# Optimization experiments

Hardware: AMD Instinct MI355X
Metric: run time of the kernel (lower is better)

## Reference

```python
import jax, jax.numpy as jnp
import numpy as np

B, D_IN, D_DENSE, S1, S2 = 16384, 1024, 1024, 1024, 1024
SPARSITY1, SPARSITY2 = 0.1, 0.01  # fraction of zeros in the 'sparse' weights


def setup_inputs() -> dict:
    key = jax.random.key(0)
    kx, k0, k1, k2, km1, km2 = jax.random.split(key, 6)
    x = jax.random.normal(kx, (B, D_IN), dtype=jnp.float32)
    # dense layer params (nn.Linear): weight [out, in], bias [out]
    w0 = jax.random.normal(k0, (D_DENSE, D_IN), dtype=jnp.float32) / np.sqrt(D_IN)
    b0 = jnp.zeros((D_DENSE,), dtype=jnp.float32)
    # sparse layers: dense randn weight elementwise-masked (mask keeps with prob 1-sparsity)
    w1 = jax.random.normal(k1, (S1, D_DENSE), dtype=jnp.float32)
    mask1 = jax.random.uniform(km1, (S1, D_DENSE)) > SPARSITY1
    b1 = jnp.zeros((S1,), dtype=jnp.float32)
    w2 = jax.random.normal(k2, (S2, S1), dtype=jnp.float32)
    mask2 = jax.random.uniform(km2, (S2, S1)) > SPARSITY2
    b2 = jnp.zeros((S2,), dtype=jnp.float32)
    return {"x": x, "w0": w0, "b0": b0, "w1": w1, "b1": b1, "mask1": mask1,
            "w2": w2, "b2": b2, "mask2": mask2}


def reference(x, w0, b0, w1, b1, mask1, w2, b2, mask2):
    # layer 1: dense linear + ReLU
    h = jax.nn.relu(jnp.einsum('bi,oi->bo', x, w0) + b0)
    # layer 2: masked ('sparse' COO in torch) linear + bias + ReLU
    h = jax.nn.relu(jnp.einsum('bi,oi->bo', h, w1 * mask1) + b1)
    # layer 3: masked linear + bias + ReLU
    out = jax.nn.relu(jnp.einsum('bi,oi->bo', h, w2 * mask2) + b2)
    return out
```

## Files before the change

### kernel.cpp

```cpp
#include <hip/hip_runtime.h>
#include <hip/hip_bf16.h>
#include <cstdint>
#include <cstddef>


typedef __bf16 bf16x8 __attribute__((ext_vector_type(8)));
typedef float  f32x4  __attribute__((ext_vector_type(4)));

#define AS1 __attribute__((address_space(1)))
#define AS3 __attribute__((address_space(3)))

__device__ __forceinline__ void gload_lds16(const void* g, void* l) {
    __builtin_amdgcn_global_load_lds((const AS1 void*)g, (AS3 void*)l, 16, 0, 0);
}

__global__ void detect_mask(const unsigned char* __restrict__ m, int* __restrict__ flag) {
    const int t = threadIdx.x;
    int or1 = 0, or3 = 0;
    for (int e = t; e < 256; e += 64) { or1 |= m[e * 4 + 1]; or3 |= m[e * 4 + 3]; }
    unsigned long long b1 = __ballot(or1 != 0);
    unsigned long long b3 = __ballot(or3 != 0);
    if (t == 0) *flag = b1 ? 1 : (b3 ? 2 : 0);
}

__device__ __forceinline__ void prep_body(const float* __restrict__ w,
                                          const void* __restrict__ mask, int mode,
                                          __bf16* __restrict__ out, long i) {
    float4 a = *reinterpret_cast<const float4*>(w + i);
    float4 b = *reinterpret_cast<const float4*>(w + i + 4);
    float v[8] = {a.x, a.y, a.z, a.w, b.x, b.y, b.z, b.w};
    if (mask) {
        if (mode == 1) {
            const unsigned char* mp = (const unsigned char*)mask;
            #pragma unroll
            for (int j = 0; j < 8; ++j) v[j] = mp[i + j] ? v[j] : 0.f;
        } else if (mode == 0) {
            const int* mp = (const int*)mask;
            #pragma unroll
            for (int j = 0; j < 8; ++j) v[j] = mp[i + j] ? v[j] : 0.f;
        } else {
            const float* mp = (const float*)mask;
            #pragma unroll
            for (int j = 0; j < 8; ++j) v[j] = (mp[i + j] != 0.f) ? v[j] : 0.f;
        }
    }
    bf16x8 o;
    #pragma unroll
    for (int j = 0; j < 8; ++j) o[j] = (__bf16)v[j];
    *reinterpret_cast<bf16x8*>(out + i) = o;
}

__global__ void prep_all(const float* __restrict__ x, __bf16* __restrict__ xb,
                         const float* __restrict__ w0, const float* __restrict__ w1,
                         const float* __restrict__ w2,
                         const void* __restrict__ m1, const void* __restrict__ m2,
                         const int* __restrict__ flag,
                         __bf16* __restrict__ w0b, __bf16* __restrict__ w1b,
                         __bf16* __restrict__ w2b) {
    const int bid = blockIdx.x;
    if (bid < 8192) {
        long i = ((long)bid * blockDim.x + threadIdx.x) * 8;
        float4 a = *reinterpret_cast<const float4*>(x + i);
        float4 b = *reinterpret_cast<const float4*>(x + i + 4);
        bf16x8 o;
        o[0] = (__bf16)a.x; o[1] = (__bf16)a.y; o[2] = (__bf16)a.z; o[3] = (__bf16)a.w;
        o[4] = (__bf16)b.x; o[5] = (__bf16)b.y; o[6] = (__bf16)b.z; o[7] = (__bf16)b.w;
        *reinterpret_cast<bf16x8*>(xb + i) = o;
    } else {
        const int q = bid - 8192, wi = q >> 9, sub = q & 511;
        long i = ((long)sub * blockDim.x + threadIdx.x) * 8;
        const int mode = *flag;
        if (wi == 0)      prep_body(w0, nullptr, mode, w0b, i);
        else if (wi == 1) prep_body(w1, m1,      mode, w1b, i);
        else              prep_body(w2, m2,      mode, w2b, i);
    }
}

__device__ __forceinline__ f32x4 mfma16(bf16x8 a, bf16x8 b, f32x4 c) {
    return __builtin_amdgcn_mfma_f32_16x16x32_bf16(a, b, c, 0, 0, 0);
}

#define MFMAQ(Q, A00, A01, A10, A11)                                        \
    __builtin_amdgcn_s_setprio(1);                                          \
    _Pragma("unroll")                                                       \
    for (int n = 0; n < 4; ++n) {                                           \
        acc[2*(Q)][n]   = mfma16(A00, b[n][0], acc[2*(Q)][n]);              \
        acc[2*(Q)][n]   = mfma16(A01, b[n][1], acc[2*(Q)][n]);              \
        acc[2*(Q)+1][n] = mfma16(A10, b[n][0], acc[2*(Q)+1][n]);            \
        acc[2*(Q)+1][n] = mfma16(A11, b[n][1], acc[2*(Q)+1][n]);            \
    }                                                                       \
    __builtin_amdgcn_s_setprio(0);

#define BAR()   __builtin_amdgcn_s_barrier(); __builtin_amdgcn_sched_barrier(0)
#define LGKM0() asm volatile("s_waitcnt lgkmcnt(0)" ::: "memory")
#define VM8()   asm volatile("s_waitcnt vmcnt(8)" ::: "memory")
#define VM0()   asm volatile("s_waitcnt vmcnt(0)" ::: "memory")

template<bool F32OUT>
__global__ __launch_bounds__(512, 2) void gemm8p(
    const __bf16* __restrict__ A, const __bf16* __restrict__ W,
    const float* __restrict__ bias,
    __bf16* __restrict__ outb, float* __restrict__ outf) {
    constexpr int NT = 16;
    extern __shared__ char smem[];

    const int t   = threadIdx.x;
    const int l   = t & 63, l15 = l & 15, lhi = l >> 4;
    const int w   = t >> 6, wr = w >> 2, wc = w & 3;

    const int bid = blockIdx.x;
    const int swz = (bid & 7) * 32 + (bid >> 3);
    const int bx = swz & 3, by = swz >> 2;
    const int brow = by * 256, bcol = bx * 256;

    const int srow = t >> 3;
    const int scol = (((t & 7) ^ ((t >> 3) & 7)) << 4) >> 1;
    const __bf16* gA = A + (size_t)(brow + srow) * 1024 + scol;
    const __bf16* gW = W + (size_t)(bcol + srow) * 1024 + scol;
    const int woff = (t & 448) * 16;

    char* const ldsA = smem;
    char* const ldsB = smem + 65536;

    auto stageAfull = [&](int d, int k0) {
        const __bf16* g = gA + k0;
        char* p = ldsA + d * 32768 + woff;
        gload_lds16(g,          p);
        gload_lds16(g + 65536,  p + 8192);
        gload_lds16(g + 131072, p + 16384);
        gload_lds16(g + 196608, p + 24576);
    };
    auto stageBh = [&](int d, int h, int k0) {
        const __bf16* g = gW + (size_t)h * 131072 + k0;
        char* p = ldsB + d * 32768 + h * 16384 + woff;
        gload_lds16(g, p);
        gload_lds16(g + 65536, p + 8192);
    };

    const int xorm  = (l & 7) << 4;
    const int koff0 = (lhi * 16) ^ xorm;
    const int koff1 = (64 + lhi * 16) ^ xorm;
    char* const aBase = ldsA + wr * 16384 + l15 * 128;
    char* const bBase = ldsB + wc * 8192 + l15 * 128;

    f32x4 acc[8][4] = {};

    stageAfull(0, 0);  stageBh(0, 0, 0);  stageBh(0, 1, 0);
    stageAfull(1, 64); stageBh(1, 0, 64); stageBh(1, 1, 64);
    VM8(); BAR();

    #pragma unroll 2
    for (int tt = 0; tt < NT; ++tt) {
        const int d  = tt & 1;
        const int k2 = (tt + 2) * 64;
        char* const aB = aBase + d * 32768;
        char* const bB = bBase + d * 32768;
        const bool st = (tt + 2 < NT);

        bf16x8 b[4][2];
        #pragma unroll
        for (int n = 0; n < 4; ++n) {
            b[n][0] = *(const bf16x8*)(bB + n * 2048 + koff0);
            b[n][1] = *(const bf16x8*)(bB + n * 2048 + koff1);
        }
        bf16x8 a00 = *(const bf16x8*)(aB + 0 * 2048 + koff0);
        bf16x8 a01 = *(const bf16x8*)(aB + 0 * 2048 + koff1);
        bf16x8 a10 = *(const bf16x8*)(aB + 1 * 2048 + koff0);
        bf16x8 a11 = *(const bf16x8*)(aB + 1 * 2048 + koff1);
        bf16x8 c00 = *(const bf16x8*)(aB + 2 * 2048 + koff0);
        bf16x8 c01 = *(const bf16x8*)(aB + 2 * 2048 + koff1);
        bf16x8 c10 = *(const bf16x8*)(aB + 3 * 2048 + koff0);
        bf16x8 c11 = *(const bf16x8*)(aB + 3 * 2048 + koff1);
        MFMAQ(0, a00, a01, a10, a11);
        LGKM0(); BAR();

        if (st) stageBh(d, 0, k2);
        a00 = *(const bf16x8*)(aB + 4 * 2048 + koff0);
        a01 = *(const bf16x8*)(aB + 4 * 2048 + koff1);
        a10 = *(const bf16x8*)(aB + 5 * 2048 + koff0);
        a11 = *(const bf16x8*)(aB + 5 * 2048 + koff1);
        MFMAQ(1, c00, c01, c10, c11);
        LGKM0(); BAR();

        if (st) stageBh(d, 1, k2);
        c00 = *(const bf16x8*)(aB + 6 * 2048 + koff0);
        c01 = *(const bf16x8*)(aB + 6 * 2048 + koff1);
        c10 = *(const bf16x8*)(aB + 7 * 2048 + koff0);
        c11 = *(const bf16x8*)(aB + 7 * 2048 + koff1);
        MFMAQ(2, a00, a01, a10, a11);
        LGKM0(); BAR();

        if (st) stageAfull(d, k2);
        MFMAQ(3, c00, c01, c10, c11);
        if (tt <= NT - 3)      { VM8(); BAR(); }
        else if (tt == NT - 2) { VM0(); BAR(); }
    }

    if constexpr (F32OUT) {
        const int orow = brow + wr * 128 + lhi * 4;
        const int ocol = bcol + wc * 64 + l15;
        #pragma unroll
        for (int n = 0; n < 4; ++n) {
            const int col = ocol + n * 16;
            const float bv = bias[col];
            #pragma unroll
            for (int m = 0; m < 8; ++m) {
                const int r0 = orow + m * 16;
                #pragma unroll
                for (int r = 0; r < 4; ++r) {
                    float v = acc[m][n][r] + bv;
                    outf[(size_t)(r0 + r) * 1024 + col] = v > 0.f ? v : 0.f;
                }
            }
        }
    } else {
        __syncthreads();
        char* const cl = smem;
        #pragma unroll
        for (int n = 0; n < 4; ++n) {
            const int colb = (wc * 64 + n * 16 + l15) * 2;
            const float bv = bias[bcol + wc * 64 + n * 16 + l15];
            #pragma unroll
            for (int m = 0; m < 8; ++m) {
                #pragma unroll
                for (int r = 0; r < 4; ++r) {
                    const int row = wr * 128 + m * 16 + lhi * 4 + r;
                    float v = acc[m][n][r] + bv;
                    v = v > 0.f ? v : 0.f;
                    *(__bf16*)(cl + row * 512 + (colb ^ ((row & 12) << 3))) = (__bf16)v;
                }
            }
        }
        __syncthreads();
        #pragma unroll
        for (int rd = 0; rd < 16; ++rd) {
            const int off = rd * 8192 + t * 16;
            const int row = off >> 9;
            const int cb  = (off & 511) ^ ((row & 12) << 3);
            bf16x8 v = *(const bf16x8*)(cl + off);
            *(bf16x8*)((char*)outb + ((size_t)(brow + row) * 1024 + bcol) * 2 + cb) = v;
        }
    }
}

extern "C" void kernel_launch(void* const* d_in, const int* in_sizes, int n_in,
                              void* d_out, int out_size, void* d_ws, size_t ws_size,
                              hipStream_t stream) {
    const float* x  = (const float*)d_in[0];
    const float* w0 = (const float*)d_in[1];
    const float* b0 = (const float*)d_in[2];
    const float* w1 = (const float*)d_in[3];
    const float* b1 = (const float*)d_in[4];
    const void*  m1 = d_in[5];
    const float* w2 = (const float*)d_in[6];
    const float* b2 = (const float*)d_in[7];
    const void*  m2 = d_in[8];
    float* out = (float*)d_out;

    char* ws = (char*)d_ws;
    __bf16* xb  = (__bf16*)(ws);
    __bf16* h1  = (__bf16*)(ws + (size_t)32 * 1024 * 1024);
    __bf16* w0b = (__bf16*)(ws + (size_t)64 * 1024 * 1024);
    __bf16* w1b = w0b + 1024 * 1024;
    __bf16* w2b = w1b + 1024 * 1024;
    int*   flag = (int*)(w2b + 1024 * 1024);

    hipFuncSetAttribute((const void*)gemm8p<false>,
                        hipFuncAttributeMaxDynamicSharedMemorySize, 131072);
    hipFuncSetAttribute((const void*)gemm8p<true>,
                        hipFuncAttributeMaxDynamicSharedMemorySize, 131072);

    detect_mask<<<1, 64, 0, stream>>>((const unsigned char*)m1, flag);
    prep_all<<<9728, 256, 0, stream>>>(x, xb, w0, w1, w2, m1, m2, flag,
                                       w0b, w1b, w2b);

    gemm8p<false><<<256, 512, 131072, stream>>>(xb, w0b, b0, h1, nullptr);
    gemm8p<false><<<256, 512, 131072, stream>>>(h1, w1b, b1, xb, nullptr);
    gemm8p<true ><<<256, 512, 131072, stream>>>(xb, w2b, b2, nullptr, out);
}
```

Measured before the change: 127.0 us.

## Prefetch next-tile LDS fragments across iterations and stage fp32 epilogue through LDS

The main loop now loads the first A fragments and first B fragment pair for the next k-tile during the last MFMA quarter of the current iteration. This hides LDS read latency at the top of each iteration, and the vmcnt wait moves earlier to make that possible. The fp32-output epilogue now writes results into swizzled LDS in two row-chunks and then stores them with coalesced float4 global writes, replacing scattered scalar stores. The cost is more live registers and extra barriers and LDS traffic in the epilogue.

```diff
diff --git a/kernel.cpp b/kernel.cpp
--- a/kernel.cpp
+++ b/kernel.cpp
@@ -84,16 +84,17 @@
     __builtin_amdgcn_s_setprio(1);                                          \
     _Pragma("unroll")                                                       \
     for (int n = 0; n < 4; ++n) {                                           \
-        acc[2*(Q)][n]   = mfma16(A00, b[n][0], acc[2*(Q)][n]);              \
-        acc[2*(Q)][n]   = mfma16(A01, b[n][1], acc[2*(Q)][n]);              \
-        acc[2*(Q)+1][n] = mfma16(A10, b[n][0], acc[2*(Q)+1][n]);            \
-        acc[2*(Q)+1][n] = mfma16(A11, b[n][1], acc[2*(Q)+1][n]);            \
+        acc[2*(Q)][n]   = mfma16(A00, bb[n][0], acc[2*(Q)][n]);             \
+        acc[2*(Q)][n]   = mfma16(A01, bb[n][1], acc[2*(Q)][n]);             \
+        acc[2*(Q)+1][n] = mfma16(A10, bb[n][0], acc[2*(Q)+1][n]);           \
+        acc[2*(Q)+1][n] = mfma16(A11, bb[n][1], acc[2*(Q)+1][n]);           \
     }                                                                       \
     __builtin_amdgcn_s_setprio(0);
 
 #define BAR()   __builtin_amdgcn_s_barrier(); __builtin_amdgcn_sched_barrier(0)
 #define LGKM0() asm volatile("s_waitcnt lgkmcnt(0)" ::: "memory")
 #define VM8()   asm volatile("s_waitcnt vmcnt(8)" ::: "memory")
+#define VM4()   asm volatile("s_waitcnt vmcnt(4)" ::: "memory")
 #define VM0()   asm volatile("s_waitcnt vmcnt(0)" ::: "memory")
 
 template<bool F32OUT>
@@ -144,33 +145,41 @@
     char* const bBase = ldsB + wc * 8192 + l15 * 128;
 
     f32x4 acc[8][4] = {};
+    bf16x8 bb[4][2], bp0, bp1;
+    bf16x8 a00, a01, a10, a11, c00, c01, c10, c11;
 
     stageAfull(0, 0);  stageBh(0, 0, 0);  stageBh(0, 1, 0);
     stageAfull(1, 64); stageBh(1, 0, 64); stageBh(1, 1, 64);
     VM8(); BAR();
+    a00 = *(const bf16x8*)(aBase + 0 * 2048 + koff0);
+    a01 = *(const bf16x8*)(aBase + 0 * 2048 + koff1);
+    a10 = *(const bf16x8*)(aBase + 1 * 2048 + koff0);
+    a11 = *(const bf16x8*)(aBase + 1 * 2048 + koff1);
+    bp0 = *(const bf16x8*)(bBase + koff0);
+    bp1 = *(const bf16x8*)(bBase + koff1);
 
     #pragma unroll 2
     for (int tt = 0; tt < NT; ++tt) {
         const int d  = tt & 1;
         const int k2 = (tt + 2) * 64;
-        char* const aB = aBase + d * 32768;
-        char* const bB = bBase + d * 32768;
+        char* const aB  = aBase + d * 32768;
+        char* const bB  = bBase + d * 32768;
+        char* const aBn = aBase + (d ^ 1) * 32768;
+        char* const bBn = bBase + (d ^ 1) * 32768;
         const bool st = (tt + 2 < NT);
-
-        bf16x8 b[4][2];
-        #pragma unroll
-        for (int n = 0; n < 4; ++n) {
-            b[n][0] = *(const bf16x8*)(bB + n * 2048 + koff0);
-            b[n][1] = *(const bf16x8*)(bB + n * 2048 + koff1);
-        }
-        bf16x8 a00 = *(const bf16x8*)(aB + 0 * 2048 + koff0);
-        bf16x8 a01 = *(const bf16x8*)(aB + 0 * 2048 + koff1);
-        bf16x8 a10 = *(const bf16x8*)(aB + 1 * 2048 + koff0);
-        bf16x8 a11 = *(const bf16x8*)(aB + 1 * 2048 + koff1);
-        bf16x8 c00 = *(const bf16x8*)(aB + 2 * 2048 + koff0);
-        bf16x8 c01 = *(const bf16x8*)(aB + 2 * 2048 + koff1);
-        bf16x8 c10 = *(const bf16x8*)(aB + 3 * 2048 + koff0);
-        bf16x8 c11 = *(const bf16x8*)(aB + 3 * 2048 + koff1);
+        const bool pf = (tt + 1 < NT);
+
+        bb[0][0] = bp0; bb[0][1] = bp1;
+        bb[1][0] = *(const bf16x8*)(bB + 1 * 2048 + koff0);
+        bb[1][1] = *(const bf16x8*)(bB + 1 * 2048 + koff1);
+        bb[2][0] = *(const bf16x8*)(bB + 2 * 2048 + koff0);
+        bb[2][1] = *(const bf16x8*)(bB + 2 * 2048 + koff1);
+        bb[3][0] = *(const bf16x8*)(bB + 3 * 2048 + koff0);
+        bb[3][1] = *(const bf16x8*)(bB + 3 * 2048 + koff1);
+        c00 = *(const bf16x8*)(aB + 2 * 2048 + koff0);
+        c01 = *(const bf16x8*)(aB + 2 * 2048 + koff1);
+        c10 = *(const bf16x8*)(aB + 3 * 2048 + koff0);
+        c11 = *(const bf16x8*)(aB + 3 * 2048 + koff1);
         MFMAQ(0, a00, a01, a10, a11);
         LGKM0(); BAR();
 
@@ -188,29 +197,54 @@
         c10 = *(const bf16x8*)(aB + 7 * 2048 + koff0);
         c11 = *(const bf16x8*)(aB + 7 * 2048 + koff1);
         MFMAQ(2, a00, a01, a10, a11);
+        if (tt <= NT - 3)      { VM4(); }
+        else if (tt == NT - 2) { VM0(); }
         LGKM0(); BAR();
 
         if (st) stageAfull(d, k2);
+        if (pf) {
+            a00 = *(const bf16x8*)(aBn + 0 * 2048 + koff0);
+            a01 = *(const bf16x8*)(aBn + 0 * 2048 + koff1);
+            a10 = *(const bf16x8*)(aBn + 1 * 2048 + koff0);
+            a11 = *(const bf16x8*)(aBn + 1 * 2048 + koff1);
+            bp0 = *(const bf16x8*)(bBn + koff0);
+            bp1 = *(const bf16x8*)(bBn + koff1);
+        }
         MFMAQ(3, c00, c01, c10, c11);
-        if (tt <= NT - 3)      { VM8(); BAR(); }
-        else if (tt == NT - 2) { VM0(); BAR(); }
+        LGKM0(); BAR();
     }
 
     if constexpr (F32OUT) {
-        const int orow = brow + wr * 128 + lhi * 4;
-        const int ocol = bcol + wc * 64 + l15;
+        char* const cl = smem;
         #pragma unroll
-        for (int n = 0; n < 4; ++n) {
-            const int col = ocol + n * 16;
-            const float bv = bias[col];
-            #pragma unroll
-            for (int m = 0; m < 8; ++m) {
-                const int r0 = orow + m * 16;
+        for (int chunk = 0; chunk < 2; ++chunk) {
+            __syncthreads();
+            if (wr == chunk) {
                 #pragma unroll
-                for (int r = 0; r < 4; ++r) {
-                    float v = acc[m][n][r] + bv;
-                    outf[(size_t)(r0 + r) * 1024 + col] = v > 0.f ? v : 0.f;
+                for (int n = 0; n < 4; ++n) {
+                    const int colb = (wc * 64 + n * 16 + l15) * 4;
+                    const float bv = bias[bcol + wc * 64 + n * 16 + l15];
+                    #pragma unroll
+                    for (int m = 0; m < 8; ++m) {
+                        #pragma unroll
+                        for (int r = 0; r < 4; ++r) {
+                            const int row = m * 16 + lhi * 4 + r;
+                            float v = acc[m][n][r] + bv;
+                            v = v > 0.f ? v : 0.f;
+                            *(float*)(cl + row * 1024 + (colb ^ ((row & 12) << 4))) = v;
+                        }
+                    }
                 }
+            }
+            __syncthreads();
+            #pragma unroll
+            for (int rd = 0; rd < 16; ++rd) {
+                const int off = rd * 8192 + t * 16;
+                const int row = off >> 10;
+                const int cb  = (off & 1023) ^ ((row & 12) << 4);
+                float4 v = *(const float4*)(cl + off);
+                *(float4*)((char*)outf +
+                           ((size_t)(brow + chunk * 128 + row) * 1024 + bcol) * 4 + cb) = v;
             }
         }
     } else {
```

Result: slower. 130.5 us (+2.8%).

## Stage fp32 epilogue through LDS for coalesced float4 stores, relax barrier scheduling

Applied to the files above, without the earlier changes.

The fp32-output epilogue no longer writes scattered 4-byte values straight from MFMA accumulators. It writes them into LDS with an XOR swizzle, one 128-row half at a time, then reads them back as contiguous float4 rows and stores those to global memory. This targets the poorly coalesced stores of the large fp32 output. The BAR macro also drops its sched_barrier, so the compiler can move instructions across barriers, at some risk of hurting the hand-tuned MFMA/load interleaving.

```diff
diff --git a/kernel.cpp b/kernel.cpp
--- a/kernel.cpp
+++ b/kernel.cpp
@@ -91,7 +91,7 @@
     }                                                                       \
     __builtin_amdgcn_s_setprio(0);
 
-#define BAR()   __builtin_amdgcn_s_barrier(); __builtin_amdgcn_sched_barrier(0)
+#define BAR()   __builtin_amdgcn_s_barrier()
 #define LGKM0() asm volatile("s_waitcnt lgkmcnt(0)" ::: "memory")
 #define VM8()   asm volatile("s_waitcnt vmcnt(8)" ::: "memory")
 #define VM0()   asm volatile("s_waitcnt vmcnt(0)" ::: "memory")
@@ -197,20 +197,36 @@
     }
 
     if constexpr (F32OUT) {
-        const int orow = brow + wr * 128 + lhi * 4;
-        const int ocol = bcol + wc * 64 + l15;
-        #pragma unroll
-        for (int n = 0; n < 4; ++n) {
-            const int col = ocol + n * 16;
-            const float bv = bias[col];
-            #pragma unroll
-            for (int m = 0; m < 8; ++m) {
-                const int r0 = orow + m * 16;
+        char* const cl = smem;
+        #pragma unroll
+        for (int chunk = 0; chunk < 2; ++chunk) {
+            __syncthreads();
+            if (wr == chunk) {
                 #pragma unroll
-                for (int r = 0; r < 4; ++r) {
-                    float v = acc[m][n][r] + bv;
-                    outf[(size_t)(r0 + r) * 1024 + col] = v > 0.f ? v : 0.f;
+                for (int n = 0; n < 4; ++n) {
+                    const int colb = (wc * 64 + n * 16 + l15) * 4;
+                    const float bv = bias[bcol + wc * 64 + n * 16 + l15];
+                    #pragma unroll
+                    for (int m = 0; m < 8; ++m) {
+                        #pragma unroll
+                        for (int r = 0; r < 4; ++r) {
+                            const int row = m * 16 + lhi * 4 + r;
+                            float v = acc[m][n][r] + bv;
+                            v = v > 0.f ? v : 0.f;
+                            *(float*)(cl + row * 1024 + (colb ^ ((row & 12) << 4))) = v;
+                        }
+                    }
                 }
+            }
+            __syncthreads();
+            #pragma unroll
+            for (int rd = 0; rd < 16; ++rd) {
+                const int off = rd * 8192 + t * 16;
+                const int row = off >> 10;
+                const int cb  = (off & 1023) ^ ((row & 12) << 4);
+                float4 v = *(const float4*)(cl + off);
+                *(float4*)((char*)outf +
+                           ((size_t)(brow + chunk * 128 + row) * 1024 + bcol) * 4 + cb) = v;
             }
         }
     } else {
```

New measurement: 130.0 us. 2.4% more time.
